# Optimization experiments

Measured on AMD Instinct MI355X. Metric: run time of the kernel, lower is better.

The kernel has to match this reference:

```python
import jax, jax.numpy as jnp
import numpy as np

NA = 100000   # authors
NP_ = 100000  # papers
D = 128       # hidden dim
H = 4         # heads
DH = 32       # head dim (D = H*DH)
L = 2         # layers
R = 3         # relations: 0=writes(a->p), 1=rev_writes(p->a), 2=cites(p->p)
E = 400000    # edges per relation
OUT = 40


def setup_inputs() -> dict:
    key = jax.random.key(0)
    ks = jax.random.split(key, 16)
    s = 0.05
    return {
        "x_author": jax.random.normal(ks[0], (NA, D), jnp.float32),
        "x_paper": jax.random.normal(ks[1], (NP_, D), jnp.float32),
        "ei_writes": jax.random.randint(ks[2], (2, E), 0, NA, dtype=jnp.int32),
        "ei_rev": jax.random.randint(ks[3], (2, E), 0, NA, dtype=jnp.int32),
        "ei_cites": jax.random.randint(ks[4], (2, E), 0, NP_, dtype=jnp.int32),
        "proj_w": jax.random.normal(ks[5], (2, D, D), jnp.float32) * s,
        "proj_b": jax.random.normal(ks[6], (2, D), jnp.float32) * s,
        "kqv_w": jax.random.normal(ks[7], (L, 3, 2, D, D), jnp.float32) * s,  # [layer, {k,q,v}, type, D, D]
        "kqv_b": jax.random.normal(ks[8], (L, 3, 2, D), jnp.float32) * s,
        "out_w": jax.random.normal(ks[9], (L, 2, D, D), jnp.float32) * s,
        "out_b": jax.random.normal(ks[10], (L, 2, D), jnp.float32) * s,
        "rel_a": jax.random.normal(ks[11], (L, R, H, DH, DH), jnp.float32) * s,
        "rel_m": jax.random.normal(ks[12], (L, R, H, DH, DH), jnp.float32) * s,
        "p_rel": jnp.ones((L, R, H), jnp.float32),
        "skip": jnp.ones((L, 2), jnp.float32),
        "cls_w": jax.random.normal(ks[13], (D, OUT), jnp.float32) * s,
        "cls_b": jnp.zeros((OUT,), jnp.float32),
    }


def _seg_softmax(sc, dst, n):
    # softmax over incoming edges grouped by destination node; sc: [E,H]
    m = jax.ops.segment_max(sc, dst, num_segments=n)
    m = jnp.where(jnp.isfinite(m), m, 0.0)
    e = jnp.exp(sc - m[dst])
    z = jax.ops.segment_sum(e, dst, num_segments=n)
    return e / (z[dst] + 1e-16)


def _hgt_layer(h_a, h_p, ei_w, ei_r, ei_c, kqv_w, kqv_b, out_w, out_b, rel_a, rel_m, p_rel, skip):
    na, npp = h_a.shape[0], h_p.shape[0]

    def kqv(h, t):
        k = (h @ kqv_w[0, t] + kqv_b[0, t]).reshape(-1, H, DH)
        q = (h @ kqv_w[1, t] + kqv_b[1, t]).reshape(-1, H, DH)
        v = (h @ kqv_w[2, t] + kqv_b[2, t]).reshape(-1, H, DH)
        return k, q, v

    k_a, q_a, v_a = kqv(h_a, 0)
    k_p, q_p, v_p = kqv(h_p, 1)
    scale = 1.0 / jnp.sqrt(jnp.float32(DH))

    def edge_msgs(k_src, v_src, q_dst, ei, r):
        ke = jnp.einsum('ehd,hdf->ehf', k_src[ei[0]], rel_a[r])
        ve = jnp.einsum('ehd,hdf->ehf', v_src[ei[0]], rel_m[r])
        sc = (q_dst[ei[1]] * ke).sum(-1) * p_rel[r] * scale  # [E,H]
        return sc, ve

    # destination = paper: writes (r=0) + cites (r=2); softmax jointly per dst node
    sc_w, ve_w = edge_msgs(k_a, v_a, q_p, ei_w, 0)
    sc_c, ve_c = edge_msgs(k_p, v_p, q_p, ei_c, 2)
    sc_p = jnp.concatenate([sc_w, sc_c], 0)
    ve_p = jnp.concatenate([ve_w, ve_c], 0)
    dst_p = jnp.concatenate([ei_w[1], ei_c[1]], 0)
    al_p = _seg_softmax(sc_p, dst_p, npp)
    agg_p = jax.ops.segment_sum(ve_p * al_p[..., None], dst_p, num_segments=npp).reshape(npp, D)

    # destination = author: rev_writes (r=1)
    sc_r, ve_r = edge_msgs(k_p, v_p, q_a, ei_r, 1)
    al_a = _seg_softmax(sc_r, ei_r[1], na)
    agg_a = jax.ops.segment_sum(ve_r * al_a[..., None], ei_r[1], num_segments=na).reshape(na, D)

    def out_mix(agg, h, t):
        o = jax.nn.gelu(agg, approximate=False) @ out_w[t] + out_b[t]
        s = jax.nn.sigmoid(skip[t])
        return s * o + (1.0 - s) * h

    # HGTNet.forward applies ELU after each HGTConv (dropout is identity in eval mode)
    h_a = jax.nn.elu(out_mix(agg_a, h_a, 0))
    h_p = jax.nn.elu(out_mix(agg_p, h_p, 1))
    return h_a, h_p


def reference(x_author, x_paper, ei_writes, ei_rev, ei_cites, proj_w, proj_b,
              kqv_w, kqv_b, out_w, out_b, rel_a, rel_m, p_rel, skip, cls_w, cls_b):
    h_a = x_author @ proj_w[0] + proj_b[0]
    h_p = x_paper @ proj_w[1] + proj_b[1]
    for l in range(L):
        h_a, h_p = _hgt_layer(h_a, h_p, ei_writes, ei_rev, ei_cites,
                              kqv_w[l], kqv_b[l], out_w[l], out_b[l],
                              rel_a[l], rel_m[l], p_rel[l], skip[l])
    return h_p @ cls_w + cls_b
```

## Files before the change

### kernel.cpp

```cpp
#include <hip/hip_runtime.h>
#include <hip/hip_bf16.h>
#include <math.h>

constexpr int NA  = 100000;
constexpr int NPP = 100000;
constexpr int D   = 128;
constexpr int H   = 4;
constexpr int E   = 400000;
constexpr int R   = 3;
constexpr int L   = 2;
constexpr int NSLOT = 23;
constexpr int SLOT_ELEMS = 8 * 4 * 512;

using s8v = __attribute__((ext_vector_type(8))) short;
using f4v = __attribute__((ext_vector_type(4))) float;
typedef unsigned short ushort_t;

static __device__ __forceinline__ unsigned short f2bf(float f) {
  unsigned u = __float_as_uint(f);
  return (unsigned short)((u + 0x7fffu + ((u >> 16) & 1u)) >> 16);
}
static __device__ __forceinline__ float bf2f(unsigned short s) {
  return __uint_as_float(((unsigned)s) << 16);
}
static __device__ __forceinline__ float klo(int i) {
  return __uint_as_float(((unsigned)i) << 16);
}
static __device__ __forceinline__ float vhi(int i) {
  return __uint_as_float(((unsigned)i) & 0xffff0000u);
}
static __device__ __forceinline__ float gelu_f(float x) {
  return 0.5f * x * (1.0f + erff(x * 0.70710678118654752f));
}
static __device__ __forceinline__ float elu_f(float x) {
  return x > 0.0f ? x : expm1f(x);
}

template<int NT16, int NCOLS, int STORE, bool GELU_A, bool MIX, bool BLO, typename TA>
__global__ __launch_bounds__(256, 4) void gemm4(
    const TA* __restrict__ A,
    const ushort_t* __restrict__ Bhi, const ushort_t* __restrict__ Blo,
    const float* __restrict__ bias, void* __restrict__ Cv,
    const float* __restrict__ skip_ptr, int M) {
  constexpr int HN = NT16 * 2048;
  __shared__ ushort_t Bs[HN * (BLO ? 2 : 1)];
  constexpr bool AFP32 = sizeof(TA) == 4;

  for (int i = threadIdx.x; i < (HN / 8) * (BLO ? 2 : 1); i += 256) {
    int half = i / (HN / 8), j = i % (HN / 8);
    const ushort_t* src = (half ? Blo : Bhi) + (size_t)j * 8;
    *(s8v*)&Bs[half * HN + j * 8] = *(const s8v*)src;
  }
  __syncthreads();

  const int lane = threadIdx.x & 63;
  const int wave = threadIdx.x >> 6;
  const int row0 = blockIdx.x * 128 + wave * 32;
  const int g = lane >> 4, li = lane & 15;

  f4v acc0[NT16], acc1[NT16];
#pragma unroll
  for (int ct = 0; ct < NT16; ++ct) {
    acc0[ct] = f4v{0.f, 0.f, 0.f, 0.f};
    acc1[ct] = f4v{0.f, 0.f, 0.f, 0.f};
  }

  int ar0 = row0 + li;       if (ar0 >= M) ar0 = M - 1;
  int ar1 = row0 + 16 + li;  if (ar1 >= M) ar1 = M - 1;

#pragma unroll
  for (int ks = 0; ks < 4; ++ks) {
    s8v ahi[2], alo[2];
#pragma unroll
    for (int rf = 0; rf < 2; ++rf) {
      int ar = rf ? ar1 : ar0;
      if constexpr (AFP32) {
        const float* ap = (const float*)A + (size_t)ar * 128 + ks * 32 + g * 4;
        float4 u0 = *(const float4*)ap;
        float4 u1 = *(const float4*)(ap + 16);
        float x[8] = {u0.x, u0.y, u0.z, u0.w, u1.x, u1.y, u1.z, u1.w};
#pragma unroll
        for (int i = 0; i < 8; ++i) {
          float v = GELU_A ? gelu_f(x[i]) : x[i];
          unsigned short h = f2bf(v);
          ahi[rf][i] = (short)h;
          alo[rf][i] = (short)f2bf(v - bf2f(h));
        }
      } else {
        const ushort_t* ap = (const ushort_t*)A + (size_t)ar * 128 + ks * 32 + g * 4;
        ushort4 u0 = *(const ushort4*)ap;
        ushort4 u1 = *(const ushort4*)(ap + 16);
        ushort_t uu[8] = {u0.x, u0.y, u0.z, u0.w, u1.x, u1.y, u1.z, u1.w};
#pragma unroll
        for (int i = 0; i < 8; ++i) {
          if (GELU_A) ahi[rf][i] = (short)f2bf(gelu_f(bf2f(uu[i])));
          else        ahi[rf][i] = (short)uu[i];
        }
      }
    }
#pragma unroll
    for (int ct = 0; ct < NT16; ++ct) {
      const ushort_t* bp = &Bs[(ct * 4 + ks) * 512 + lane * 8];
      s8v bhi = *(const s8v*)bp;
      acc0[ct] = __builtin_amdgcn_mfma_f32_16x16x32_bf16(ahi[0], bhi, acc0[ct], 0, 0, 0);
      acc1[ct] = __builtin_amdgcn_mfma_f32_16x16x32_bf16(ahi[1], bhi, acc1[ct], 0, 0, 0);
      if constexpr (BLO) {
        s8v blo = *(const s8v*)(bp + HN);
        if constexpr (AFP32) {
          acc0[ct] = __builtin_amdgcn_mfma_f32_16x16x32_bf16(alo[0], bhi, acc0[ct], 0, 0, 0);
          acc1[ct] = __builtin_amdgcn_mfma_f32_16x16x32_bf16(alo[1], bhi, acc1[ct], 0, 0, 0);
        }
        acc0[ct] = __builtin_amdgcn_mfma_f32_16x16x32_bf16(ahi[0], blo, acc0[ct], 0, 0, 0);
        acc1[ct] = __builtin_amdgcn_mfma_f32_16x16x32_bf16(ahi[1], blo, acc1[ct], 0, 0, 0);
      }
    }
  }

  float sskip = 0.f;
  if (MIX) sskip = 1.f / (1.f + __expf(-*skip_ptr));
#pragma unroll
  for (int rf = 0; rf < 2; ++rf) {
#pragma unroll
    for (int ct = 0; ct < NT16; ++ct) {
      int col = ct * 16 + li;
      bool colok = (col < NCOLS);
      float bv = colok ? bias[col] : 0.f;
      f4v a = rf ? acc1[ct] : acc0[ct];
#pragma unroll
      for (int r = 0; r < 4; ++r) {
        int grow = row0 + rf * 16 + g * 4 + r;
        if (grow < M && colok) {
          float v = a[r] + bv;
          size_t off = (size_t)grow * NCOLS + col;
          if constexpr (MIX) {
            ushort_t* Cp = (ushort_t*)Cv;
            float hprev = bf2f(Cp[off]);
            Cp[off] = f2bf(elu_f(sskip * v + (1.f - sskip) * hprev));
          } else if constexpr (STORE == 1) {
            ((ushort_t*)Cv)[off] = f2bf(v);
          } else {
            ((float*)Cv)[off] = v;
          }
        }
      }
    }
  }
}

__global__ __launch_bounds__(256, 4) void gemm_kv(
    const ushort_t* __restrict__ A,
    const ushort_t* __restrict__ Bhi, const ushort_t* __restrict__ Blo,
    const float* __restrict__ bias, ushort_t* __restrict__ kvout, int M) {
  __shared__ ushort_t Bs[16384];
  const int ch = blockIdx.y;
  for (int i = threadIdx.x; i < 2048; i += 256) {
    int kvh = i >> 10, j = i & 1023;
    const ushort_t* src = Bhi + (size_t)kvh * SLOT_ELEMS + ch * 8192 + j * 8;
    *(s8v*)&Bs[kvh * 8192 + j * 8] = *(const s8v*)src;
  }
  __syncthreads();

  const int lane = threadIdx.x & 63;
  const int wave = threadIdx.x >> 6;
  const int row0 = blockIdx.x * 128 + wave * 32;
  const int g = lane >> 4, li = lane & 15;

  f4v acc0[8], acc1[8];
#pragma unroll
  for (int t = 0; t < 8; ++t) {
    acc0[t] = f4v{0.f, 0.f, 0.f, 0.f};
    acc1[t] = f4v{0.f, 0.f, 0.f, 0.f};
  }

  int ar0 = row0 + li;       if (ar0 >= M) ar0 = M - 1;
  int ar1 = row0 + 16 + li;  if (ar1 >= M) ar1 = M - 1;

#pragma unroll
  for (int ks = 0; ks < 4; ++ks) {
    s8v a0, a1;
    {
      const ushort_t* ap = A + (size_t)ar0 * 128 + ks * 32 + g * 4;
      ushort4 u0 = *(const ushort4*)ap;
      ushort4 u1 = *(const ushort4*)(ap + 16);
      a0[0] = (short)u0.x; a0[1] = (short)u0.y; a0[2] = (short)u0.z; a0[3] = (short)u0.w;
      a0[4] = (short)u1.x; a0[5] = (short)u1.y; a0[6] = (short)u1.z; a0[7] = (short)u1.w;
    }
    {
      const ushort_t* ap = A + (size_t)ar1 * 128 + ks * 32 + g * 4;
      ushort4 u0 = *(const ushort4*)ap;
      ushort4 u1 = *(const ushort4*)(ap + 16);
      a1[0] = (short)u0.x; a1[1] = (short)u0.y; a1[2] = (short)u0.z; a1[3] = (short)u0.w;
      a1[4] = (short)u1.x; a1[5] = (short)u1.y; a1[6] = (short)u1.z; a1[7] = (short)u1.w;
    }
#pragma unroll
    for (int t = 0; t < 4; ++t) {
      s8v kh = *(const s8v*)&Bs[(t * 4 + ks) * 512 + lane * 8];
      acc0[t] = __builtin_amdgcn_mfma_f32_16x16x32_bf16(a0, kh, acc0[t], 0, 0, 0);
      acc1[t] = __builtin_amdgcn_mfma_f32_16x16x32_bf16(a1, kh, acc1[t], 0, 0, 0);
      s8v vh = *(const s8v*)&Bs[8192 + (t * 4 + ks) * 512 + lane * 8];
      acc0[4 + t] = __builtin_amdgcn_mfma_f32_16x16x32_bf16(a0, vh, acc0[4 + t], 0, 0, 0);
      acc1[4 + t] = __builtin_amdgcn_mfma_f32_16x16x32_bf16(a1, vh, acc1[4 + t], 0, 0, 0);
    }
  }

#pragma unroll
  for (int rf = 0; rf < 2; ++rf) {
#pragma unroll
    for (int t = 0; t < 4; ++t) {
      int col = ch * 64 + t * 16 + li;
      float bk = bias[col], bv = bias[128 + col];
#pragma unroll
      for (int r = 0; r < 4; ++r) {
        int grow = row0 + rf * 16 + g * 4 + r;
        if (grow < M) {
          float kvl = rf ? acc1[t][r] : acc0[t][r];
          float vvl = rf ? acc1[4 + t][r] : acc0[4 + t][r];
          ushort2 o;
          o.x = f2bf(kvl + bk);
          o.y = f2bf(vvl + bv);
          *(ushort2*)(kvout + (size_t)grow * 256 + 2 * col) = o;
        }
      }
    }
  }
}

__global__ __launch_bounds__(256, 4) void gemm_qkv(
    const ushort_t* __restrict__ Aq, const ushort_t* __restrict__ Akv,
    const ushort_t* __restrict__ Bq, const ushort_t* __restrict__ Bkv,
    const float* __restrict__ bias_q, const float* __restrict__ bias_kv,
    ushort_t* __restrict__ qout, ushort_t* __restrict__ kvout, int M) {
  __shared__ ushort_t Bs[16384];
  const int lane = threadIdx.x & 63;
  const int wave = threadIdx.x >> 6;
  const int row0 = blockIdx.x * 128 + wave * 32;
  const int g = lane >> 4, li = lane & 15;

  if (blockIdx.y == 0) {
    for (int i = threadIdx.x; i < 2048; i += 256)
      *(s8v*)&Bs[i * 8] = *(const s8v*)(Bq + (size_t)i * 8);
    __syncthreads();
    f4v acc0[8], acc1[8];
#pragma unroll
    for (int ct = 0; ct < 8; ++ct) {
      acc0[ct] = f4v{0.f, 0.f, 0.f, 0.f};
      acc1[ct] = f4v{0.f, 0.f, 0.f, 0.f};
    }
    int ar0 = row0 + li;       if (ar0 >= M) ar0 = M - 1;
    int ar1 = row0 + 16 + li;  if (ar1 >= M) ar1 = M - 1;
#pragma unroll
    for (int ks = 0; ks < 4; ++ks) {
      s8v a0, a1;
      {
        const ushort_t* ap = Aq + (size_t)ar0 * 128 + ks * 32 + g * 4;
        ushort4 u0 = *(const ushort4*)ap;
        ushort4 u1 = *(const ushort4*)(ap + 16);
        a0[0]=(short)u0.x; a0[1]=(short)u0.y; a0[2]=(short)u0.z; a0[3]=(short)u0.w;
        a0[4]=(short)u1.x; a0[5]=(short)u1.y; a0[6]=(short)u1.z; a0[7]=(short)u1.w;
      }
      {
        const ushort_t* ap = Aq + (size_t)ar1 * 128 + ks * 32 + g * 4;
        ushort4 u0 = *(const ushort4*)ap;
        ushort4 u1 = *(const ushort4*)(ap + 16);
        a1[0]=(short)u0.x; a1[1]=(short)u0.y; a1[2]=(short)u0.z; a1[3]=(short)u0.w;
        a1[4]=(short)u1.x; a1[5]=(short)u1.y; a1[6]=(short)u1.z; a1[7]=(short)u1.w;
      }
#pragma unroll
      for (int ct = 0; ct < 8; ++ct) {
        s8v bhi = *(const s8v*)&Bs[(ct * 4 + ks) * 512 + lane * 8];
        acc0[ct] = __builtin_amdgcn_mfma_f32_16x16x32_bf16(a0, bhi, acc0[ct], 0, 0, 0);
        acc1[ct] = __builtin_amdgcn_mfma_f32_16x16x32_bf16(a1, bhi, acc1[ct], 0, 0, 0);
      }
    }
#pragma unroll
    for (int rf = 0; rf < 2; ++rf) {
#pragma unroll
      for (int ct = 0; ct < 8; ++ct) {
        int col = ct * 16 + li;
        float bv = bias_q[col];
        f4v a = rf ? acc1[ct] : acc0[ct];
#pragma unroll
        for (int r = 0; r < 4; ++r) {
          int grow = row0 + rf * 16 + g * 4 + r;
          if (grow < M) qout[(size_t)grow * 128 + col] = f2bf(a[r] + bv);
        }
      }
    }
  } else {
    const int ch = blockIdx.y - 1;
    for (int i = threadIdx.x; i < 2048; i += 256) {
      int kvh = i >> 10, j = i & 1023;
      const ushort_t* src = Bkv + (size_t)kvh * SLOT_ELEMS + ch * 8192 + j * 8;
      *(s8v*)&Bs[kvh * 8192 + j * 8] = *(const s8v*)src;
    }
    __syncthreads();
    f4v acc0[8], acc1[8];
#pragma unroll
    for (int t = 0; t < 8; ++t) {
      acc0[t] = f4v{0.f, 0.f, 0.f, 0.f};
      acc1[t] = f4v{0.f, 0.f, 0.f, 0.f};
    }
    int ar0 = row0 + li;       if (ar0 >= M) ar0 = M - 1;
    int ar1 = row0 + 16 + li;  if (ar1 >= M) ar1 = M - 1;
#pragma unroll
    for (int ks = 0; ks < 4; ++ks) {
      s8v a0, a1;
      {
        const ushort_t* ap = Akv + (size_t)ar0 * 128 + ks * 32 + g * 4;
        ushort4 u0 = *(const ushort4*)ap;
        ushort4 u1 = *(const ushort4*)(ap + 16);
        a0[0]=(short)u0.x; a0[1]=(short)u0.y; a0[2]=(short)u0.z; a0[3]=(short)u0.w;
        a0[4]=(short)u1.x; a0[5]=(short)u1.y; a0[6]=(short)u1.z; a0[7]=(short)u1.w;
      }
      {
        const ushort_t* ap = Akv + (size_t)ar1 * 128 + ks * 32 + g * 4;
        ushort4 u0 = *(const ushort4*)ap;
        ushort4 u1 = *(const ushort4*)(ap + 16);
        a1[0]=(short)u0.x; a1[1]=(short)u0.y; a1[2]=(short)u0.z; a1[3]=(short)u0.w;
        a1[4]=(short)u1.x; a1[5]=(short)u1.y; a1[6]=(short)u1.z; a1[7]=(short)u1.w;
      }
#pragma unroll
      for (int t = 0; t < 4; ++t) {
        s8v kh = *(const s8v*)&Bs[(t * 4 + ks) * 512 + lane * 8];
        acc0[t] = __builtin_amdgcn_mfma_f32_16x16x32_bf16(a0, kh, acc0[t], 0, 0, 0);
        acc1[t] = __builtin_amdgcn_mfma_f32_16x16x32_bf16(a1, kh, acc1[t], 0, 0, 0);
        s8v vh = *(const s8v*)&Bs[8192 + (t * 4 + ks) * 512 + lane * 8];
        acc0[4 + t] = __builtin_amdgcn_mfma_f32_16x16x32_bf16(a0, vh, acc0[4 + t], 0, 0, 0);
        acc1[4 + t] = __builtin_amdgcn_mfma_f32_16x16x32_bf16(a1, vh, acc1[4 + t], 0, 0, 0);
      }
    }
#pragma unroll
    for (int rf = 0; rf < 2; ++rf) {
#pragma unroll
      for (int t = 0; t < 4; ++t) {
        int col = ch * 64 + t * 16 + li;
        float bk = bias_kv[col], bv = bias_kv[128 + col];
#pragma unroll
        for (int r = 0; r < 4; ++r) {
          int grow = row0 + rf * 16 + g * 4 + r;
          if (grow < M) {
            float kvl = rf ? acc1[t][r] : acc0[t][r];
            float vvl = rf ? acc1[4 + t][r] : acc0[4 + t][r];
            ushort2 o;
            o.x = f2bf(kvl + bk);
            o.y = f2bf(vvl + bv);
            *(ushort2*)(kvout + (size_t)grow * 256 + 2 * col) = o;
          }
        }
      }
    }
  }
}

__global__ __launch_bounds__(256) void combine_w(
    const float* __restrict__ kqv_w, const float* __restrict__ kqv_b,
    const float* __restrict__ rel_a, const float* __restrict__ rel_m,
    float* __restrict__ cw, float* __restrict__ cb) {
  int b  = blockIdx.x;
  int kv = b & 1;
  int r  = (b >> 1) % R;
  int l  = b / (2 * R);
  int t_src = (r == 0) ? 0 : 1;
// ... 126 lines not shown
  __shared__ int sm[256];
  sm[threadIdx.x] = s; __syncthreads();
  for (int o = 1; o < 256; o <<= 1) {
    int x = (threadIdx.x >= o) ? sm[threadIdx.x - o] : 0;
    __syncthreads(); sm[threadIdx.x] += x; __syncthreads();
  }
  int run = boffv + sm[threadIdx.x] - s;
  if (ok) {
    int w[16];
#pragma unroll
    for (int i = 0; i < 16; ++i) { w[i] = run; run += v[i]; }
#pragma unroll
    for (int i4 = 0; i4 < 4; ++i4) *(int4*)(rp + base + i4 * 4) = *(const int4*)&w[i4*4];
  }
  if (t25 == 24 && threadIdx.x == 255) rpb[NPP] = boffv + sm[255];
}

template<bool TWO>
__global__ __launch_bounds__(256, 8) void attn6(
    const int* __restrict__ rp1, const int* __restrict__ col1,
    const ushort_t* __restrict__ kv1,
    const int* __restrict__ rp2, const int* __restrict__ col2,
    const ushort_t* __restrict__ kv2,
    const ushort_t* __restrict__ q,
    const float* __restrict__ prel1, const float* __restrict__ prel2,
    int ndst, ushort_t* __restrict__ aggout) {
  int lane = threadIdx.x & 63;
  int wave = threadIdx.x >> 6;
  int half = lane >> 5;
  int l32  = lane & 31;
  int dst  = blockIdx.x * 8 + wave * 2 + half;
  int head = l32 >> 3;
  const float scale = 0.17677669529663688f;
  float pr1 = prel1[head] * scale;
  float pr2 = TWO ? prel2[head] * scale : pr1;
  ushort4 qv = *(const ushort4*)(q + (size_t)dst * D + l32 * 4);
  float q0 = bf2f(qv.x), q1 = bf2f(qv.y), q2 = bf2f(qv.z), q3 = bf2f(qv.w);
  int e0a = rp1[dst];
  int d1  = rp1[dst + 1] - e0a;
  int e0b = 0, dt = d1;
  if (TWO) { e0b = rp2[dst]; dt = d1 + (rp2[dst + 1] - e0b); }
  float z = 0.f, a0 = 0.f, a1 = 0.f, a2 = 0.f, a3 = 0.f;
  for (int jj = 0; jj < dt; jj += 4) {
    int4 us[4]; bool vs[4]; float prs[4];
#pragma unroll
    for (int s2 = 0; s2 < 4; ++s2) {
      int idx = jj + s2;
      bool v = idx < dt;
      bool f = (!TWO) || (idx < d1);
      int ci = 0;
      if (v) ci = f ? (e0a + idx) : (e0b + idx - d1);
      int src = f ? col1[ci] : col2[ci];
      const ushort_t* kvp = f ? kv1 : kv2;
      us[s2] = *(const int4*)(kvp + (size_t)src * 256 + l32 * 8);
      vs[s2] = v;
      prs[s2] = f ? pr1 : pr2;
    }
#pragma unroll
    for (int s2 = 0; s2 < 4; ++s2) {
      float p = q0 * klo(us[s2].x) + q1 * klo(us[s2].y)
              + q2 * klo(us[s2].z) + q3 * klo(us[s2].w);
      p += __shfl_xor(p, 1);
      p += __shfl_xor(p, 2);
      p += __shfl_xor(p, 4);
      float e = vs[s2] ? __expf(p * prs[s2]) : 0.f;
      z  += e;
      a0 += e * vhi(us[s2].x);
      a1 += e * vhi(us[s2].y);
      a2 += e * vhi(us[s2].z);
      a3 += e * vhi(us[s2].w);
    }
  }
  float inv = 1.f / (z + 1e-16f);
  ushort4 o;
  o.x = f2bf(a0 * inv);
  o.y = f2bf(a1 * inv);
  o.z = f2bf(a2 * inv);
  o.w = f2bf(a3 * inv);
  *(ushort4*)(aggout + (size_t)dst * D + l32 * 4) = o;
}

extern "C" void kernel_launch(void* const* d_in, const int* in_sizes, int n_in,
                              void* d_out, int out_size, void* d_ws, size_t ws_size,
                              hipStream_t stream) {
  const float* x_a    = (const float*)d_in[0];
  const float* x_p    = (const float*)d_in[1];
  const int*   ei_w   = (const int*)d_in[2];
  const int*   ei_r   = (const int*)d_in[3];
  const int*   ei_c   = (const int*)d_in[4];
  const float* proj_w = (const float*)d_in[5];
  const float* proj_b = (const float*)d_in[6];
  const float* kqv_w  = (const float*)d_in[7];
  const float* kqv_b  = (const float*)d_in[8];
  const float* out_w  = (const float*)d_in[9];
// ... 1 lines not shown
  const float* rel_a  = (const float*)d_in[11];
  const float* rel_m  = (const float*)d_in[12];
  const float* p_rel  = (const float*)d_in[13];
  const float* skip   = (const float*)d_in[14];
  const float* cls_w  = (const float*)d_in[15];
  const float* cls_b  = (const float*)d_in[16];
  float* out = (float*)d_out;

  const size_t NF = (size_t)NA * D;
  float* ws    = (float*)d_ws;
  float* cw    = ws;
  float* cb    = cw + 12 * D * D;
  ushort_t* h_a   = (ushort_t*)(cb + 12 * D);
  ushort_t* h_p   = h_a + NF;
  ushort_t* b_q   = h_p + NF;
  ushort_t* b_kv  = b_q + NF;
  ushort_t* b_kv2 = b_kv + 2 * NF;
  ushort_t* phi   = b_kv2 + 2 * NF;
  ushort_t* plo   = phi + (size_t)NSLOT * SLOT_ELEMS;
  int* ip    = (int*)(plo + (size_t)NSLOT * SLOT_ELEMS);
  int* rp_w  = ip;
  int* rp_c  = rp_w + (NPP + 1);
  int* rp_r  = rp_c + (NPP + 1);
  int* degz  = rp_r + (NA + 1);
  int* cntz  = degz + 3 * NPP;
  int* colz  = cntz + 3 * NPP;
  int* bsum  = colz + 3 * E;
  int* boff  = bsum + 128;
  size_t need_bytes = (size_t)((char*)(boff + 128) - (char*)d_ws);
  if (ws_size < need_bytes) return;

  hipMemsetAsync(degz, 0, sizeof(int) * 6 * (size_t)NPP, stream);

  count3<<<dim3(256, 3), 256, 0, stream>>>(ei_w, ei_c, ei_r, degz);
  scan_partial<<<75, 256, 0, stream>>>(degz, bsum);
  scan_final<<<75, 256, 0, stream>>>(degz, bsum, rp_w, rp_c, rp_r);
  fill3<<<dim3(256, 3), 256, 0, stream>>>(ei_w, ei_c, ei_r, rp_w, rp_c, rp_r, cntz, colz);
  int* col_w = colz;
  int* col_c = colz + E;
  int* col_r = colz + 2 * E;

  combine_w<<<12, 256, 0, stream>>>(kqv_w, kqv_b, rel_a, rel_m, cw, cb);
  pack_b<<<NSLOT, 256, 0, stream>>>(proj_w, kqv_w, out_w, cls_w, cw, phi, plo);

  auto PH = [&](int s){ return phi + (size_t)s * SLOT_ELEMS; };
  auto PL = [&](int s){ return plo + (size_t)s * SLOT_ELEMS; };

  const int GB2 = (NA + 127) / 128;
  const int GA  = NA / 8;
  const dim3 G1(GB2, 1), GKV(GB2, 2), GQKV(GB2, 3);
  gemm4<8, 128, 1, false, false, true, float><<<G1, 256, 0, stream>>>(
      x_a, PH(0), PL(0), proj_b,     h_a, nullptr, NA);
  gemm4<8, 128, 1, false, false, true, float><<<G1, 256, 0, stream>>>(
      x_p, PH(1), PL(1), proj_b + D, h_p, nullptr, NPP);

  for (int l = 0; l < L; ++l) {
    const int SQA = 2 + l * 10 + 0, SQP = 2 + l * 10 + 1;
    auto SKV = [&](int r){ return 2 + l * 10 + 2 + r * 2; };
    const int SO0 = 2 + l * 10 + 8, SO1 = 2 + l * 10 + 9;
    const float* bq_a = kqv_b + ((size_t)((l*3 + 1)*2 + 0)) * D;
    const float* bq_p = kqv_b + ((size_t)((l*3 + 1)*2 + 1)) * D;
    auto CB2 = [&](int r){ return cb + ((size_t)((l*R + r)*2)) * D; };
    const float* prelW = p_rel + (size_t)(l*R + 0) * H;
    const float* prelR = p_rel + (size_t)(l*R + 1) * H;
    const float* prelC = p_rel + (size_t)(l*R + 2) * H;

    gemm_qkv<<<GQKV, 256, 0, stream>>>(
        h_a, h_p, PH(SQA), PH(SKV(1)), bq_a, CB2(1), b_q, b_kv, NA);
    attn6<false><<<GA, 256, 0, stream>>>(
        rp_r, col_r, b_kv, nullptr, nullptr, nullptr,
        b_q, prelR, prelR, NA, b_q);
    gemm_kv<<<GKV, 256, 0, stream>>>(
        h_a, PH(SKV(0)), PL(SKV(0)), CB2(0), b_kv2, NA);
    gemm4<8, 128, 1, true, true, false, ushort_t><<<G1, 256, 0, stream>>>(
        b_q, PH(SO0), PL(SO0), out_b + (size_t)(l*2 + 0) * D, h_a,
        skip + l*2 + 0, NA);

    gemm_qkv<<<GQKV, 256, 0, stream>>>(
        h_p, h_p, PH(SQP), PH(SKV(2)), bq_p, CB2(2), b_q, b_kv, NPP);
    attn6<true><<<GA, 256, 0, stream>>>(
        rp_w, col_w, b_kv2, rp_c, col_c, b_kv,
        b_q, prelW, prelC, NPP, b_q);
    gemm4<8, 128, 1, true, true, false, ushort_t><<<G1, 256, 0, stream>>>(
        b_q, PH(SO1), PL(SO1), out_b + (size_t)(l*2 + 1) * D, h_p,
        skip + l*2 + 1, NPP);
  }

  gemm4<3, 40, 0, false, false, true, ushort_t><<<G1, 256, 0, stream>>>(
      h_p, PH(22), PL(22), cls_b, out, nullptr, NPP);
}
```

Before: 895.3 us.

## Merge independent GEMM and attention launches into combined heterogeneous kernels

The per-layer sequence of separate launches is regrouped into combined kernels. One kernel interleaves the author-side attention blocks with the writes-relation K/V GEMM blocks in a single grid, and another runs the author output-mix GEMM alongside the paper Q and cites K/V GEMMs, with a second Q buffer added to remove the conflict. This cuts launch count and serialization and lets independent work fill the GPU together. In exchange, blocks of different shapes share one kernel: the attention blocks now run under a 4-wave-per-SIMD launch bound instead of 8 and carry an unused 32 KB LDS allocation, which may reduce attention occupancy.

```diff
diff --git a/kernel.cpp b/kernel.cpp
--- a/kernel.cpp
+++ b/kernel.cpp
@@ -11,6 +11,9 @@
 constexpr int L   = 2;
 constexpr int NSLOT = 23;
 constexpr int SLOT_ELEMS = 8 * 4 * 512;
+constexpr int GB2c = (NA + 127) / 128;
+constexpr int GAc  = NA / 8;
+constexpr int MEGA_G = 1564 * 9;
 
 using s8v = __attribute__((ext_vector_type(8))) short;
 using f4v = __attribute__((ext_vector_type(4))) float;
@@ -36,38 +39,302 @@
   return x > 0.0f ? x : expm1f(x);
 }
 
-template<int NT16, int NCOLS, int STORE, bool GELU_A, bool MIX, bool BLO, typename TA>
+static __device__ __forceinline__ void load_a2(
+    const ushort_t* __restrict__ A, int ar0, int ar1, int ks, int g,
+    s8v& a0, s8v& a1) {
+  const ushort_t* ap0 = A + (size_t)ar0 * 128 + ks * 32 + g * 4;
+  ushort4 u0 = *(const ushort4*)ap0;
+  ushort4 u1 = *(const ushort4*)(ap0 + 16);
+  a0[0]=(short)u0.x; a0[1]=(short)u0.y; a0[2]=(short)u0.z; a0[3]=(short)u0.w;
+  a0[4]=(short)u1.x; a0[5]=(short)u1.y; a0[6]=(short)u1.z; a0[7]=(short)u1.w;
+  const ushort_t* ap1 = A + (size_t)ar1 * 128 + ks * 32 + g * 4;
+  ushort4 v0 = *(const ushort4*)ap1;
+  ushort4 v1 = *(const ushort4*)(ap1 + 16);
+  a1[0]=(short)v0.x; a1[1]=(short)v0.y; a1[2]=(short)v0.z; a1[3]=(short)v0.w;
+  a1[4]=(short)v1.x; a1[5]=(short)v1.y; a1[6]=(short)v1.z; a1[7]=(short)v1.w;
+}
+
+template<bool GELU_A, bool MIX>
+__device__ __forceinline__ void dev_gemm8(
+    const ushort_t* __restrict__ A, const ushort_t* __restrict__ Bhi,
+    const float* __restrict__ bias, ushort_t* __restrict__ Cout,
+    const float* __restrict__ skip_ptr, int M, int bx, ushort_t* Bs) {
+  for (int i = threadIdx.x; i < 2048; i += 256)
+    *(s8v*)&Bs[i * 8] = *(const s8v*)(Bhi + (size_t)i * 8);
+  __syncthreads();
+  const int lane = threadIdx.x & 63;
+  const int wave = threadIdx.x >> 6;
+  const int row0 = bx * 128 + wave * 32;
+  const int g = lane >> 4, li = lane & 15;
+  f4v acc0[8], acc1[8];
+#pragma unroll
+  for (int ct = 0; ct < 8; ++ct) {
+    acc0[ct] = f4v{0.f, 0.f, 0.f, 0.f};
+    acc1[ct] = f4v{0.f, 0.f, 0.f, 0.f};
+  }
+  int ar0 = row0 + li;       if (ar0 >= M) ar0 = M - 1;
+  int ar1 = row0 + 16 + li;  if (ar1 >= M) ar1 = M - 1;
+#pragma unroll
+  for (int ks = 0; ks < 4; ++ks) {
+    s8v a0, a1;
+    load_a2(A, ar0, ar1, ks, g, a0, a1);
+    if (GELU_A) {
+#pragma unroll
+      for (int i = 0; i < 8; ++i) {
+        a0[i] = (short)f2bf(gelu_f(bf2f((unsigned short)a0[i])));
+        a1[i] = (short)f2bf(gelu_f(bf2f((unsigned short)a1[i])));
+      }
+    }
+#pragma unroll
+    for (int ct = 0; ct < 8; ++ct) {
+      s8v bhi = *(const s8v*)&Bs[(ct * 4 + ks) * 512 + lane * 8];
+      acc0[ct] = __builtin_amdgcn_mfma_f32_16x16x32_bf16(a0, bhi, acc0[ct], 0, 0, 0);
+      acc1[ct] = __builtin_amdgcn_mfma_f32_16x16x32_bf16(a1, bhi, acc1[ct], 0, 0, 0);
+    }
+  }
+  float sskip = 0.f;
+  if (MIX) sskip = 1.f / (1.f + __expf(-*skip_ptr));
+#pragma unroll
+  for (int rf = 0; rf < 2; ++rf) {
+#pragma unroll
+    for (int ct = 0; ct < 8; ++ct) {
+      int col = ct * 16 + li;
+      float bv = bias[col];
+      f4v a = rf ? acc1[ct] : acc0[ct];
+#pragma unroll
+      for (int r = 0; r < 4; ++r) {
+        int grow = row0 + rf * 16 + g * 4 + r;
+        if (grow < M) {
+          float v = a[r] + bv;
+          size_t off = (size_t)grow * 128 + col;
+          if constexpr (MIX) {
+            float hprev = bf2f(Cout[off]);
+            Cout[off] = f2bf(elu_f(sskip * v + (1.f - sskip) * hprev));
+          } else {
+            Cout[off] = f2bf(v);
+          }
+        }
+      }
+    }
+  }
+}
+
+__device__ __forceinline__ void dev_gemm_kv(
+    const ushort_t* __restrict__ A, const ushort_t* __restrict__ Bkv,
+    const float* __restrict__ bias, ushort_t* __restrict__ kvout,
+    int M, int bx, int ch, ushort_t* Bs) {
+  for (int i = threadIdx.x; i < 2048; i += 256) {
+    int kvh = i >> 10, j = i & 1023;
+    const ushort_t* src = Bkv + (size_t)kvh * SLOT_ELEMS + ch * 8192 + j * 8;
+    *(s8v*)&Bs[kvh * 8192 + j * 8] = *(const s8v*)src;
+  }
+  __syncthreads();
+  const int lane = threadIdx.x & 63;
+  const int wave = threadIdx.x >> 6;
+  const int row0 = bx * 128 + wave * 32;
+  const int g = lane >> 4, li = lane & 15;
+  f4v acc0[8], acc1[8];
+#pragma unroll
+  for (int t = 0; t < 8; ++t) {
+    acc0[t] = f4v{0.f, 0.f, 0.f, 0.f};
+    acc1[t] = f4v{0.f, 0.f, 0.f, 0.f};
+  }
+  int ar0 = row0 + li;       if (ar0 >= M) ar0 = M - 1;
+  int ar1 = row0 + 16 + li;  if (ar1 >= M) ar1 = M - 1;
+#pragma unroll
+  for (int ks = 0; ks < 4; ++ks) {
+    s8v a0, a1;
+    load_a2(A, ar0, ar1, ks, g, a0, a1);
+#pragma unroll
+    for (int t = 0; t < 4; ++t) {
+      s8v kh = *(const s8v*)&Bs[(t * 4 + ks) * 512 + lane * 8];
+      acc0[t] = __builtin_amdgcn_mfma_f32_16x16x32_bf16(a0, kh, acc0[t], 0, 0, 0);
+      acc1[t] = __builtin_amdgcn_mfma_f32_16x16x32_bf16(a1, kh, acc1[t], 0, 0, 0);
+      s8v vh = *(const s8v*)&Bs[8192 + (t * 4 + ks) * 512 + lane * 8];
+      acc0[4 + t] = __builtin_amdgcn_mfma_f32_16x16x32_bf16(a0, vh, acc0[4 + t], 0, 0, 0);
+      acc1[4 + t] = __builtin_amdgcn_mfma_f32_16x16x32_bf16(a1, vh, acc1[4 + t], 0, 0, 0);
+    }
+  }
+#pragma unroll
+  for (int rf = 0; rf < 2; ++rf) {
+#pragma unroll
+    for (int t = 0; t < 4; ++t) {
+      int col = ch * 64 + t * 16 + li;
+      float bk = bias[col], bv = bias[128 + col];
+#pragma unroll
+      for (int r = 0; r < 4; ++r) {
+        int grow = row0 + rf * 16 + g * 4 + r;
+        if (grow < M) {
+          float kvl = rf ? acc1[t][r] : acc0[t][r];
+          float vvl = rf ? acc1[4 + t][r] : acc0[4 + t][r];
+          ushort2 o;
+          o.x = f2bf(kvl + bk);
+          o.y = f2bf(vvl + bv);
+          *(ushort2*)(kvout + (size_t)grow * 256 + 2 * col) = o;
+        }
+      }
+    }
+  }
+}
+
+template<bool TWO>
+__device__ __forceinline__ void dev_attn(
+    const int* __restrict__ rp1, const int* __restrict__ col1,
+    const ushort_t* __restrict__ kv1,
+    const int* __restrict__ rp2, const int* __restrict__ col2,
+    const ushort_t* __restrict__ kv2,
+    const ushort_t* __restrict__ q,
+    const float* __restrict__ prel1, const float* __restrict__ prel2,
+    ushort_t* __restrict__ aggout, int ablk) {
+  int lane = threadIdx.x & 63;
+  int wave = threadIdx.x >> 6;
+  int half = lane >> 5;
+  int l32  = lane & 31;
+  int dst  = ablk * 8 + wave * 2 + half;
+  int head = l32 >> 3;
+  const float scale = 0.17677669529663688f;
+  float pr1 = prel1[head] * scale;
+  float pr2 = TWO ? prel2[head] * scale : pr1;
+  ushort4 qv = *(const ushort4*)(q + (size_t)dst * D + l32 * 4);
+  float q0 = bf2f(qv.x), q1 = bf2f(qv.y), q2 = bf2f(qv.z), q3 = bf2f(qv.w);
+  int e0a = rp1[dst];
+  int d1  = rp1[dst + 1] - e0a;
+  int e0b = 0, dt = d1;
+  if (TWO) { e0b = rp2[dst]; dt = d1 + (rp2[dst + 1] - e0b); }
+  float z = 0.f, a0 = 0.f, a1 = 0.f, a2 = 0.f, a3 = 0.f;
+  for (int jj = 0; jj < dt; jj += 4) {
+    int4 us[4]; bool vs[4]; float prs[4];
+#pragma unroll
+    for (int s2 = 0; s2 < 4; ++s2) {
+      int idx = jj + s2;
+      bool v = idx < dt;
+      bool f = (!TWO) || (idx < d1);
+      int ci = 0;
+      if (v) ci = f ? (e0a + idx) : (e0b + idx - d1);
+      int src = f ? col1[ci] : col2[ci];
+      const ushort_t* kvp = f ? kv1 : kv2;
+      us[s2] = *(const int4*)(kvp + (size_t)src * 256 + l32 * 8);
+      vs[s2] = v;
+      prs[s2] = f ? pr1 : pr2;
+    }
+#pragma unroll
+    for (int s2 = 0; s2 < 4; ++s2) {
+      float p = q0 * klo(us[s2].x) + q1 * klo(us[s2].y)
+              + q2 * klo(us[s2].z) + q3 * klo(us[s2].w);
+      p += __shfl_xor(p, 1);
+      p += __shfl_xor(p, 2);
+      p += __shfl_xor(p, 4);
+      float e = vs[s2] ? __expf(p * prs[s2]) : 0.f;
+      z  += e;
+      a0 += e * vhi(us[s2].x);
+      a1 += e * vhi(us[s2].y);
+      a2 += e * vhi(us[s2].z);
+      a3 += e * vhi(us[s2].w);
+    }
+  }
+  float inv = 1.f / (z + 1e-16f);
+  ushort4 o;
+  o.x = f2bf(a0 * inv);
+  o.y = f2bf(a1 * inv);
+  o.z = f2bf(a2 * inv);
+  o.w = f2bf(a3 * inv);
+  *(ushort4*)(aggout + (size_t)dst * D + l32 * 4) = o;
+}
+
+__global__ __launch_bounds__(256, 8) void attn_p(
+    const int* __restrict__ rp1, const int* __restrict__ col1,
+    const ushort_t* __restrict__ kv1,
+    const int* __restrict__ rp2, const int* __restrict__ col2,
+    const ushort_t* __restrict__ kv2,
+    const ushort_t* __restrict__ q,
+    const float* __restrict__ prel1, const float* __restrict__ prel2,
+    ushort_t* __restrict__ aggout) {
+  dev_attn<true>(rp1, col1, kv1, rp2, col2, kv2, q, prel1, prel2, aggout, blockIdx.x);
+}
+
+__global__ __launch_bounds__(256, 4) void mega0(
+    const int* __restrict__ rp_r, const int* __restrict__ col_r,
+    const ushort_t* __restrict__ kv1, const ushort_t* __restrict__ q,
+    const float* __restrict__ prelR, ushort_t* __restrict__ aggout,
+    const ushort_t* __restrict__ h_a, const ushort_t* __restrict__ Bkv0,
+    const float* __restrict__ cb0, ushort_t* __restrict__ kv2out) {
+  __shared__ ushort_t Bs[16384];
+  unsigned gidx = blockIdx.x;
+  if (gidx % 9 == 0) {
+    int gb = gidx / 9;
+    dev_gemm_kv(h_a, Bkv0, cb0, kv2out, NA, gb >> 1, gb & 1, Bs);
+  } else {
+    int ablk = gidx - gidx / 9 - 1;
+    if (ablk < GAc)
+      dev_attn<false>(rp_r, col_r, kv1, nullptr, nullptr, nullptr,
+                      q, prelR, prelR, aggout, ablk);
+  }
+}
+
+__global__ __launch_bounds__(256, 4) void fusedA(
+    const ushort_t* __restrict__ agg_a, const ushort_t* __restrict__ Bout,
+    const float* __restrict__ out_b0, ushort_t* __restrict__ h_a,
+    const float* __restrict__ skip0,
+    const ushort_t* __restrict__ h_p, const ushort_t* __restrict__ Bq,
+    const float* __restrict__ bq_p, ushort_t* __restrict__ qout,
+    const ushort_t* __restrict__ Bkv, const float* __restrict__ cb2,
+    ushort_t* __restrict__ kvout) {
+  __shared__ ushort_t Bs[16384];
+  if (blockIdx.y == 0) {
+    dev_gemm8<true, true>(agg_a, Bout, out_b0, h_a, skip0, NA, blockIdx.x, Bs);
+  } else if (blockIdx.y == 1) {
+    dev_gemm8<false, false>(h_p, Bq, bq_p, qout, nullptr, NPP, blockIdx.x, Bs);
+  } else {
+    dev_gemm_kv(h_p, Bkv, cb2, kvout, NPP, blockIdx.x, blockIdx.y - 2, Bs);
+  }
+}
+
+__global__ __launch_bounds__(256, 4) void gemm_qkv(
+    const ushort_t* __restrict__ Aq, const ushort_t* __restrict__ Akv,
+    const ushort_t* __restrict__ Bq, const ushort_t* __restrict__ Bkv,
+    const float* __restrict__ bias_q, const float* __restrict__ bias_kv,
+    ushort_t* __restrict__ qout, ushort_t* __restrict__ kvout, int M) {
+  __shared__ ushort_t Bs[16384];
+  if (blockIdx.y == 0)
+    dev_gemm8<false, false>(Aq, Bq, bias_q, qout, nullptr, M, blockIdx.x, Bs);
+  else
+    dev_gemm_kv(Akv, Bkv, bias_kv, kvout, M, blockIdx.x, blockIdx.y - 1, Bs);
+}
+
+__global__ __launch_bounds__(256, 4) void outmix(
+    const ushort_t* __restrict__ agg, const ushort_t* __restrict__ Bout,
+    const float* __restrict__ out_b1, ushort_t* __restrict__ h,
+    const float* __restrict__ skip1, int M) {
+  __shared__ ushort_t Bs[16384];
+  dev_gemm8<true, true>(agg, Bout, out_b1, h, skip1, M, blockIdx.x, Bs);
+}
+
+template<int NT16, int NCOLS, int STORE, bool BLO, typename TA>
 __global__ __launch_bounds__(256, 4) void gemm4(
     const TA* __restrict__ A,
     const ushort_t* __restrict__ Bhi, const ushort_t* __restrict__ Blo,
-    const float* __restrict__ bias, void* __restrict__ Cv,
-    const float* __restrict__ skip_ptr, int M) {
+    const float* __restrict__ bias, void* __restrict__ Cv, int M) {
   constexpr int HN = NT16 * 2048;
   __shared__ ushort_t Bs[HN * (BLO ? 2 : 1)];
   constexpr bool AFP32 = sizeof(TA) == 4;
-
   for (int i = threadIdx.x; i < (HN / 8) * (BLO ? 2 : 1); i += 256) {
     int half = i / (HN / 8), j = i % (HN / 8);
     const ushort_t* src = (half ? Blo : Bhi) + (size_t)j * 8;
     *(s8v*)&Bs[half * HN + j * 8] = *(const s8v*)src;
   }
   __syncthreads();
-
   const int lane = threadIdx.x & 63;
   const int wave = threadIdx.x >> 6;
   const int row0 = blockIdx.x * 128 + wave * 32;
   const int g = lane >> 4, li = lane & 15;
-
   f4v acc0[NT16], acc1[NT16];
 #pragma unroll
   for (int ct = 0; ct < NT16; ++ct) {
     acc0[ct] = f4v{0.f, 0.f, 0.f, 0.f};
     acc1[ct] = f4v{0.f, 0.f, 0.f, 0.f};
   }
-
   int ar0 = row0 + li;       if (ar0 >= M) ar0 = M - 1;
   int ar1 = row0 + 16 + li;  if (ar1 >= M) ar1 = M - 1;
-
 #pragma unroll
   for (int ks = 0; ks < 4; ++ks) {
     s8v ahi[2], alo[2];
@@ -81,21 +348,16 @@
         float x[8] = {u0.x, u0.y, u0.z, u0.w, u1.x, u1.y, u1.z, u1.w};
 #pragma unroll
         for (int i = 0; i < 8; ++i) {
-          float v = GELU_A ? gelu_f(x[i]) : x[i];
-          unsigned short h = f2bf(v);
+          unsigned short h = f2bf(x[i]);
           ahi[rf][i] = (short)h;
-          alo[rf][i] = (short)f2bf(v - bf2f(h));
+          alo[rf][i] = (short)f2bf(x[i] - bf2f(h));
         }
       } else {
         const ushort_t* ap = (const ushort_t*)A + (size_t)ar * 128 + ks * 32 + g * 4;
         ushort4 u0 = *(const ushort4*)ap;
         ushort4 u1 = *(const ushort4*)(ap + 16);
-        ushort_t uu[8] = {u0.x, u0.y, u0.z, u0.w, u1.x, u1.y, u1.z, u1.w};
-#pragma unroll
-        for (int i = 0; i < 8; ++i) {
-          if (GELU_A) ahi[rf][i] = (short)f2bf(gelu_f(bf2f(uu[i])));
-          else        ahi[rf][i] = (short)uu[i];
-        }
+        ahi[rf][0]=(short)u0.x; ahi[rf][1]=(short)u0.y; ahi[rf][2]=(short)u0.z; ahi[rf][3]=(short)u0.w;
+        ahi[rf][4]=(short)u1.x; ahi[rf][5]=(short)u1.y; ahi[rf][6]=(short)u1.z; ahi[rf][7]=(short)u1.w;
       }
     }
 #pragma unroll
@@ -115,9 +377,6 @@
       }
     }
   }
-
-  float sskip = 0.f;
-  if (MIX) sskip = 1.f / (1.f + __expf(-*skip_ptr));
 #pragma unroll
   for (int rf = 0; rf < 2; ++rf) {
 #pragma unroll
@@ -132,220 +391,8 @@
         if (grow < M && colok) {
           float v = a[r] + bv;
           size_t off = (size_t)grow * NCOLS + col;
-          if constexpr (MIX) {
-            ushort_t* Cp = (ushort_t*)Cv;
-            float hprev = bf2f(Cp[off]);
-            Cp[off] = f2bf(elu_f(sskip * v + (1.f - sskip) * hprev));
-          } else if constexpr (STORE == 1) {
-            ((ushort_t*)Cv)[off] = f2bf(v);
-          } else {
-            ((float*)Cv)[off] = v;
-          }
-        }
-      }
-    }
-  }
-}
-
-__global__ __launch_bounds__(256, 4) void gemm_kv(
-    const ushort_t* __restrict__ A,
-    const ushort_t* __restrict__ Bhi, const ushort_t* __restrict__ Blo,
-    const float* __restrict__ bias, ushort_t* __restrict__ kvout, int M) {
-  __shared__ ushort_t Bs[16384];
-  const int ch = blockIdx.y;
-  for (int i = threadIdx.x; i < 2048; i += 256) {
-    int kvh = i >> 10, j = i & 1023;
-    const ushort_t* src = Bhi + (size_t)kvh * SLOT_ELEMS + ch * 8192 + j * 8;
-    *(s8v*)&Bs[kvh * 8192 + j * 8] = *(const s8v*)src;
-  }
-  __syncthreads();
-
-  const int lane = threadIdx.x & 63;
-  const int wave = threadIdx.x >> 6;
-  const int row0 = blockIdx.x * 128 + wave * 32;
-  const int g = lane >> 4, li = lane & 15;
-
-  f4v acc0[8], acc1[8];
-#pragma unroll
-  for (int t = 0; t < 8; ++t) {
-    acc0[t] = f4v{0.f, 0.f, 0.f, 0.f};
-    acc1[t] = f4v{0.f, 0.f, 0.f, 0.f};
-  }
-
-  int ar0 = row0 + li;       if (ar0 >= M) ar0 = M - 1;
-  int ar1 = row0 + 16 + li;  if (ar1 >= M) ar1 = M - 1;
-
-#pragma unroll
-  for (int ks = 0; ks < 4; ++ks) {
-    s8v a0, a1;
-    {
-      const ushort_t* ap = A + (size_t)ar0 * 128 + ks * 32 + g * 4;
-      ushort4 u0 = *(const ushort4*)ap;
-      ushort4 u1 = *(const ushort4*)(ap + 16);
-      a0[0] = (short)u0.x; a0[1] = (short)u0.y; a0[2] = (short)u0.z; a0[3] = (short)u0.w;
-      a0[4] = (short)u1.x; a0[5] = (short)u1.y; a0[6] = (short)u1.z; a0[7] = (short)u1.w;
-    }
-    {
-      const ushort_t* ap = A + (size_t)ar1 * 128 + ks * 32 + g * 4;
-      ushort4 u0 = *(const ushort4*)ap;
-      ushort4 u1 = *(const ushort4*)(ap + 16);
-      a1[0] = (short)u0.x; a1[1] = (short)u0.y; a1[2] = (short)u0.z; a1[3] = (short)u0.w;
-      a1[4] = (short)u1.x; a1[5] = (short)u1.y; a1[6] = (short)u1.z; a1[7] = (short)u1.w;
-    }
-#pragma unroll
-    for (int t = 0; t < 4; ++t) {
-      s8v kh = *(const s8v*)&Bs[(t * 4 + ks) * 512 + lane * 8];
-      acc0[t] = __builtin_amdgcn_mfma_f32_16x16x32_bf16(a0, kh, acc0[t], 0, 0, 0);
-      acc1[t] = __builtin_amdgcn_mfma_f32_16x16x32_bf16(a1, kh, acc1[t], 0, 0, 0);
-      s8v vh = *(const s8v*)&Bs[8192 + (t * 4 + ks) * 512 + lane * 8];
-      acc0[4 + t] = __builtin_amdgcn_mfma_f32_16x16x32_bf16(a0, vh, acc0[4 + t], 0, 0, 0);
-      acc1[4 + t] = __builtin_amdgcn_mfma_f32_16x16x32_bf16(a1, vh, acc1[4 + t], 0, 0, 0);
-    }
-  }
-
-#pragma unroll
-  for (int rf = 0; rf < 2; ++rf) {
-#pragma unroll
-    for (int t = 0; t < 4; ++t) {
-      int col = ch * 64 + t * 16 + li;
-      float bk = bias[col], bv = bias[128 + col];
-#pragma unroll
-      for (int r = 0; r < 4; ++r) {
-        int grow = row0 + rf * 16 + g * 4 + r;
-        if (grow < M) {
-          float kvl = rf ? acc1[t][r] : acc0[t][r];
-          float vvl = rf ? acc1[4 + t][r] : acc0[4 + t][r];
-          ushort2 o;
-          o.x = f2bf(kvl + bk);
-          o.y = f2bf(vvl + bv);
-          *(ushort2*)(kvout + (size_t)grow * 256 + 2 * col) = o;
-        }
-      }
-    }
-  }
-}
-
-__global__ __launch_bounds__(256, 4) void gemm_qkv(
-    const ushort_t* __restrict__ Aq, const ushort_t* __restrict__ Akv,
-    const ushort_t* __restrict__ Bq, const ushort_t* __restrict__ Bkv,
-    const float* __restrict__ bias_q, const float* __restrict__ bias_kv,
-    ushort_t* __restrict__ qout, ushort_t* __restrict__ kvout, int M) {
-  __shared__ ushort_t Bs[16384];
-  const int lane = threadIdx.x & 63;
-  const int wave = threadIdx.x >> 6;
-  const int row0 = blockIdx.x * 128 + wave * 32;
-  const int g = lane >> 4, li = lane & 15;
-
-  if (blockIdx.y == 0) {
-    for (int i = threadIdx.x; i < 2048; i += 256)
-      *(s8v*)&Bs[i * 8] = *(const s8v*)(Bq + (size_t)i * 8);
-    __syncthreads();
-    f4v acc0[8], acc1[8];
-#pragma unroll
-    for (int ct = 0; ct < 8; ++ct) {
-      acc0[ct] = f4v{0.f, 0.f, 0.f, 0.f};
-      acc1[ct] = f4v{0.f, 0.f, 0.f, 0.f};
-    }
-    int ar0 = row0 + li;       if (ar0 >= M) ar0 = M - 1;
-    int ar1 = row0 + 16 + li;  if (ar1 >= M) ar1 = M - 1;
-#pragma unroll
-    for (int ks = 0; ks < 4; ++ks) {
-      s8v a0, a1;
-      {
-        const ushort_t* ap = Aq + (size_t)ar0 * 128 + ks * 32 + g * 4;
-        ushort4 u0 = *(const ushort4*)ap;
-        ushort4 u1 = *(const ushort4*)(ap + 16);
-        a0[0]=(short)u0.x; a0[1]=(short)u0.y; a0[2]=(short)u0.z; a0[3]=(short)u0.w;
-        a0[4]=(short)u1.x; a0[5]=(short)u1.y; a0[6]=(short)u1.z; a0[7]=(short)u1.w;
-      }
-      {
-        const ushort_t* ap = Aq + (size_t)ar1 * 128 + ks * 32 + g * 4;
-        ushort4 u0 = *(const ushort4*)ap;
-        ushort4 u1 = *(const ushort4*)(ap + 16);
-        a1[0]=(short)u0.x; a1[1]=(short)u0.y; a1[2]=(short)u0.z; a1[3]=(short)u0.w;
-        a1[4]=(short)u1.x; a1[5]=(short)u1.y; a1[6]=(short)u1.z; a1[7]=(short)u1.w;
-      }
-#pragma unroll
-      for (int ct = 0; ct < 8; ++ct) {
-        s8v bhi = *(const s8v*)&Bs[(ct * 4 + ks) * 512 + lane * 8];
-        acc0[ct] = __builtin_amdgcn_mfma_f32_16x16x32_bf16(a0, bhi, acc0[ct], 0, 0, 0);
-        acc1[ct] = __builtin_amdgcn_mfma_f32_16x16x32_bf16(a1, bhi, acc1[ct], 0, 0, 0);
-      }
-    }
-#pragma unroll
-    for (int rf = 0; rf < 2; ++rf) {
-#pragma unroll
-      for (int ct = 0; ct < 8; ++ct) {
-        int col = ct * 16 + li;
-        float bv = bias_q[col];
-        f4v a = rf ? acc1[ct] : acc0[ct];
-#pragma unroll
-        for (int r = 0; r < 4; ++r) {
-          int grow = row0 + rf * 16 + g * 4 + r;
-          if (grow < M) qout[(size_t)grow * 128 + col] = f2bf(a[r] + bv);
-        }
-      }
-    }
-  } else {
-    const int ch = blockIdx.y - 1;
-    for (int i = threadIdx.x; i < 2048; i += 256) {
-      int kvh = i >> 10, j = i & 1023;
-      const ushort_t* src = Bkv + (size_t)kvh * SLOT_ELEMS + ch * 8192 + j * 8;
-      *(s8v*)&Bs[kvh * 8192 + j * 8] = *(const s8v*)src;
-    }
-    __syncthreads();
-    f4v acc0[8], acc1[8];
-#pragma unroll
-    for (int t = 0; t < 8; ++t) {
-      acc0[t] = f4v{0.f, 0.f, 0.f, 0.f};
-      acc1[t] = f4v{0.f, 0.f, 0.f, 0.f};
-    }
-    int ar0 = row0 + li;       if (ar0 >= M) ar0 = M - 1;
-    int ar1 = row0 + 16 + li;  if (ar1 >= M) ar1 = M - 1;
-#pragma unroll
-    for (int ks = 0; ks < 4; ++ks) {
-      s8v a0, a1;
-      {
-        const ushort_t* ap = Akv + (size_t)ar0 * 128 + ks * 32 + g * 4;
-        ushort4 u0 = *(const ushort4*)ap;
-        ushort4 u1 = *(const ushort4*)(ap + 16);
-        a0[0]=(short)u0.x; a0[1]=(short)u0.y; a0[2]=(short)u0.z; a0[3]=(short)u0.w;
-        a0[4]=(short)u1.x; a0[5]=(short)u1.y; a0[6]=(short)u1.z; a0[7]=(short)u1.w;
-      }
-      {
-        const ushort_t* ap = Akv + (size_t)ar1 * 128 + ks * 32 + g * 4;
-        ushort4 u0 = *(const ushort4*)ap;
-        ushort4 u1 = *(const ushort4*)(ap + 16);
-        a1[0]=(short)u0.x; a1[1]=(short)u0.y; a1[2]=(short)u0.z; a1[3]=(short)u0.w;
-        a1[4]=(short)u1.x; a1[5]=(short)u1.y; a1[6]=(short)u1.z; a1[7]=(short)u1.w;
-      }
-#pragma unroll
-      for (int t = 0; t < 4; ++t) {
-        s8v kh = *(const s8v*)&Bs[(t * 4 + ks) * 512 + lane * 8];
-        acc0[t] = __builtin_amdgcn_mfma_f32_16x16x32_bf16(a0, kh, acc0[t], 0, 0, 0);
-        acc1[t] = __builtin_amdgcn_mfma_f32_16x16x32_bf16(a1, kh, acc1[t], 0, 0, 0);
-        s8v vh = *(const s8v*)&Bs[8192 + (t * 4 + ks) * 512 + lane * 8];
-        acc0[4 + t] = __builtin_amdgcn_mfma_f32_16x16x32_bf16(a0, vh, acc0[4 + t], 0, 0, 0);
-        acc1[4 + t] = __builtin_amdgcn_mfma_f32_16x16x32_bf16(a1, vh, acc1[4 + t], 0, 0, 0);
-      }
-    }
-#pragma unroll
-    for (int rf = 0; rf < 2; ++rf) {
-#pragma unroll
-      for (int t = 0; t < 4; ++t) {
-        int col = ch * 64 + t * 16 + li;
-        float bk = bias_kv[col], bv = bias_kv[128 + col];
-#pragma unroll
-        for (int r = 0; r < 4; ++r) {
-          int grow = row0 + rf * 16 + g * 4 + r;
-          if (grow < M) {
-            float kvl = rf ? acc1[t][r] : acc0[t][r];
-            float vvl = rf ? acc1[4 + t][r] : acc0[4 + t][r];
-            ushort2 o;
-            o.x = f2bf(kvl + bk);
-            o.y = f2bf(vvl + bv);
-            *(ushort2*)(kvout + (size_t)grow * 256 + 2 * col) = o;
-          }
+          if constexpr (STORE == 1) ((ushort_t*)Cv)[off] = f2bf(v);
+          else                      ((float*)Cv)[off] = v;
         }
       }
     }
@@ -502,70 +549,6 @@
     for (int i4 = 0; i4 < 4; ++i4) *(int4*)(rp + base + i4 * 4) = *(const int4*)&w[i4*4];
   }
   if (t25 == 24 && threadIdx.x == 255) rpb[NPP] = boffv + sm[255];
-}
-
-template<bool TWO>
-__global__ __launch_bounds__(256, 8) void attn6(
-    const int* __restrict__ rp1, const int* __restrict__ col1,
-    const ushort_t* __restrict__ kv1,
-    const int* __restrict__ rp2, const int* __restrict__ col2,
-    const ushort_t* __restrict__ kv2,
-    const ushort_t* __restrict__ q,
-    const float* __restrict__ prel1, const float* __restrict__ prel2,
-    int ndst, ushort_t* __restrict__ aggout) {
-  int lane = threadIdx.x & 63;
-  int wave = threadIdx.x >> 6;
-  int half = lane >> 5;
-  int l32  = lane & 31;
-  int dst  = blockIdx.x * 8 + wave * 2 + half;
-  int head = l32 >> 3;
-  const float scale = 0.17677669529663688f;
-  float pr1 = prel1[head] * scale;
-  float pr2 = TWO ? prel2[head] * scale : pr1;
-  ushort4 qv = *(const ushort4*)(q + (size_t)dst * D + l32 * 4);
-  float q0 = bf2f(qv.x), q1 = bf2f(qv.y), q2 = bf2f(qv.z), q3 = bf2f(qv.w);
-  int e0a = rp1[dst];
-  int d1  = rp1[dst + 1] - e0a;
-  int e0b = 0, dt = d1;
-  if (TWO) { e0b = rp2[dst]; dt = d1 + (rp2[dst + 1] - e0b); }
-  float z = 0.f, a0 = 0.f, a1 = 0.f, a2 = 0.f, a3 = 0.f;
-  for (int jj = 0; jj < dt; jj += 4) {
-    int4 us[4]; bool vs[4]; float prs[4];
-#pragma unroll
-    for (int s2 = 0; s2 < 4; ++s2) {
-      int idx = jj + s2;
-      bool v = idx < dt;
-      bool f = (!TWO) || (idx < d1);
-      int ci = 0;
-      if (v) ci = f ? (e0a + idx) : (e0b + idx - d1);
-      int src = f ? col1[ci] : col2[ci];
-      const ushort_t* kvp = f ? kv1 : kv2;
-      us[s2] = *(const int4*)(kvp + (size_t)src * 256 + l32 * 8);
-      vs[s2] = v;
-      prs[s2] = f ? pr1 : pr2;
-    }
-#pragma unroll
-    for (int s2 = 0; s2 < 4; ++s2) {
-      float p = q0 * klo(us[s2].x) + q1 * klo(us[s2].y)
-              + q2 * klo(us[s2].z) + q3 * klo(us[s2].w);
-      p += __shfl_xor(p, 1);
-      p += __shfl_xor(p, 2);
-      p += __shfl_xor(p, 4);
-      float e = vs[s2] ? __expf(p * prs[s2]) : 0.f;
-      z  += e;
-      a0 += e * vhi(us[s2].x);
-      a1 += e * vhi(us[s2].y);
-      a2 += e * vhi(us[s2].z);
-      a3 += e * vhi(us[s2].w);
-    }
-  }
-  float inv = 1.f / (z + 1e-16f);
-  ushort4 o;
-  o.x = f2bf(a0 * inv);
-  o.y = f2bf(a1 * inv);
-  o.z = f2bf(a2 * inv);
-  o.w = f2bf(a3 * inv);
-  *(ushort4*)(aggout + (size_t)dst * D + l32 * 4) = o;
 }
 
 extern "C" void kernel_launch(void* const* d_in, const int* in_sizes, int n_in,
@@ -597,7 +580,8 @@
   ushort_t* h_a   = (ushort_t*)(cb + 12 * D);
   ushort_t* h_p   = h_a + NF;
   ushort_t* b_q   = h_p + NF;
-  ushort_t* b_kv  = b_q + NF;
+  ushort_t* b_q2  = b_q + NF;
+  ushort_t* b_kv  = b_q2 + NF;
   ushort_t* b_kv2 = b_kv + 2 * NF;
   ushort_t* phi   = b_kv2 + 2 * NF;
   ushort_t* plo   = phi + (size_t)NSLOT * SLOT_ELEMS;
@@ -609,8 +593,7 @@
   int* cntz  = degz + 3 * NPP;
   int* colz  = cntz + 3 * NPP;
   int* bsum  = colz + 3 * E;
-  int* boff  = bsum + 128;
-  size_t need_bytes = (size_t)((char*)(boff + 128) - (char*)d_ws);
+  size_t need_bytes = (size_t)((char*)(bsum + 128) - (char*)d_ws);
   if (ws_size < need_bytes) return;
 
   hipMemsetAsync(degz, 0, sizeof(int) * 6 * (size_t)NPP, stream);
@@ -629,13 +612,11 @@
   auto PH = [&](int s){ return phi + (size_t)s * SLOT_ELEMS; };
   auto PL = [&](int s){ return plo + (size_t)s * SLOT_ELEMS; };
 
-  const int GB2 = (NA + 127) / 128;
-  const int GA  = NA / 8;
-  const dim3 G1(GB2, 1), GKV(GB2, 2), GQKV(GB2, 3);
-  gemm4<8, 128, 1, false, false, true, float><<<G1, 256, 0, stream>>>(
-      x_a, PH(0), PL(0), proj_b,     h_a, nullptr, NA);
-  gemm4<8, 128, 1, false, false, true, float><<<G1, 256, 0, stream>>>(
-      x_p, PH(1), PL(1), proj_b + D, h_p, nullptr, NPP);
+  const dim3 G1(GB2c, 1), GQKV(GB2c, 3), GF(GB2c, 4);
+  gemm4<8, 128, 1, true, float><<<G1, 256, 0, stream>>>(
+      x_a, PH(0), PL(0), proj_b,     h_a, NA);
+  gemm4<8, 128, 1, true, float><<<G1, 256, 0, stream>>>(
+      x_p, PH(1), PL(1), proj_b + D, h_p, NPP);
 
   for (int l = 0; l < L; ++l) {
     const int SQA = 2 + l * 10 + 0, SQP = 2 + l * 10 + 1;
@@ -650,25 +631,20 @@
 
     gemm_qkv<<<GQKV, 256, 0, stream>>>(
         h_a, h_p, PH(SQA), PH(SKV(1)), bq_a, CB2(1), b_q, b_kv, NA);
-    attn6<false><<<GA, 256, 0, stream>>>(
-        rp_r, col_r, b_kv, nullptr, nullptr, nullptr,
-        b_q, prelR, prelR, NA, b_q);
-    gemm_kv<<<GKV, 256, 0, stream>>>(
-        h_a, PH(SKV(0)), PL(SKV(0)), CB2(0), b_kv2, NA);
-    gemm4<8, 128, 1, true, true, false, ushort_t><<<G1, 256, 0, stream>>>(
-        b_q, PH(SO0), PL(SO0), out_b + (size_t)(l*2 + 0) * D, h_a,
-        skip + l*2 + 0, NA);
-
-    gemm_qkv<<<GQKV, 256, 0, stream>>>(
-        h_p, h_p, PH(SQP), PH(SKV(2)), bq_p, CB2(2), b_q, b_kv, NPP);
-    attn6<true><<<GA, 256, 0, stream>>>(
+    mega0<<<MEGA_G, 256, 0, stream>>>(
+        rp_r, col_r, b_kv, b_q, prelR, b_q,
+        h_a, PH(SKV(0)), CB2(0), b_kv2);
+    fusedA<<<GF, 256, 0, stream>>>(
+        b_q, PH(SO0), out_b + (size_t)(l*2 + 0) * D, h_a, skip + l*2 + 0,
+        h_p, PH(SQP), bq_p, b_q2,
+        PH(SKV(2)), CB2(2), b_kv);
+    attn_p<<<GAc, 256, 0, stream>>>(
         rp_w, col_w, b_kv2, rp_c, col_c, b_kv,
-        b_q, prelW, prelC, NPP, b_q);
-    gemm4<8, 128, 1, true, true, false, ushort_t><<<G1, 256, 0, stream>>>(
-        b_q, PH(SO1), PL(SO1), out_b + (size_t)(l*2 + 1) * D, h_p,
-        skip + l*2 + 1, NPP);
-  }
-
-  gemm4<3, 40, 0, false, false, true, ushort_t><<<G1, 256, 0, stream>>>(
-      h_p, PH(22), PL(22), cls_b, out, nullptr, NPP);
-}
+        b_q2, prelW, prelC, b_q2);
+    outmix<<<G1, 256, 0, stream>>>(
+        b_q2, PH(SO1), out_b + (size_t)(l*2 + 1) * D, h_p, skip + l*2 + 1, NPP);
+  }
+
+  gemm4<3, 40, 0, true, ushort_t><<<G1, 256, 0, stream>>>(
+      h_p, PH(22), PL(22), cls_b, out, NPP);
+}
```

Result: faster. 875.8 us (-2.2%).
